# Performance work log

Measured on AMD Instinct MI355X. Metric: run time of the kernel, lower is better.

The kernel has to match this reference:

```python
import jax, jax.numpy as jnp
import numpy as np

O_DIM, A_DIM, Z_DIM = 256, 8, 9
D, H, L, M, B = 128, 128, 4, 4, 65536  # module dim, MLP hidden, n_layers, n_modules, batch


def setup_inputs() -> dict:
    key = jax.random.key(0)
    ks = jax.random.split(key, 18)
    s = 0.05
    return {
        "o": jax.random.normal(ks[0], (B, O_DIM), jnp.float32),
        "z_map": jax.random.uniform(ks[1], (B, Z_DIM), jnp.float32),
        "collision_prob": jax.random.uniform(ks[2], (B, 1), jnp.float32),
        # base obs embedding and routing (task) embedding
        "Wb": jax.random.normal(ks[3], (O_DIM, D), jnp.float32) * s,
        "bb": jnp.zeros((D,), jnp.float32),
        "Wz": jax.random.normal(ks[4], (Z_DIM + 1, D), jnp.float32) * s,
        "bz": jnp.zeros((D,), jnp.float32),
        # L layers x M modules of DxD linears
        "Wm": jax.random.normal(ks[5], (L, M, D, D), jnp.float32) * s,
        "bm": jnp.zeros((L, M, D), jnp.float32),
        # routing heads: L-1 inter-layer (M*M) gates + final (M,) gate
        "Wg": jax.random.normal(ks[6], (L - 1, D, M * M), jnp.float32) * s,
        "Wg_last": jax.random.normal(ks[7], (D, M), jnp.float32) * s,
        # dueling heads
        "Wv": jax.random.normal(ks[8], (D, 1), jnp.float32) * s,
        "bv": jnp.zeros((1,), jnp.float32),
        "Wa1": jax.random.normal(ks[9], (D, H), jnp.float32) * s,
        "ba1": jnp.zeros((H,), jnp.float32),
        "Wa2": jax.random.normal(ks[10], (H, A_DIM), jnp.float32) * s,
        "ba2": jnp.zeros((A_DIM,), jnp.float32),
    }


def _softmodule(o, z_map, collision_prob, Wb, bb, Wz, bz, Wm, bm, Wg, Wg_last):
    f0 = jax.nn.relu(o @ Wb + bb)                              # (B, D)
    z_in = jnp.concatenate([z_map, collision_prob], axis=-1)   # (B, Z+1)
    g = jax.nn.relu(z_in @ Wz + bz) * f0                       # routing embedding (B, D)
    # layer 0: all modules consume the obs embedding
    x = jax.nn.relu(jnp.einsum("bd,mde->bme", f0, Wm[0]) + bm[0])  # (B, M, D)
    for l in range(1, L):
        logits = (g @ Wg[l - 1]).reshape(-1, M, M)             # (B, i, j)
        p = jax.nn.softmax(logits, axis=1)                     # soft routing over incoming modules i
        xin = jnp.einsum("bij,bid->bjd", p, x)                 # weighted gather-combine
        x = jax.nn.relu(jnp.einsum("bmd,mde->bme", xin, Wm[l]) + bm[l])
    p_last = jax.nn.softmax(g @ Wg_last, axis=-1)              # (B, M)
    return jnp.einsum("bm,bmd->bd", p_last, x)                 # (B, D)


def reference(o, z_map, collision_prob, Wb, bb, Wz, bz, Wm, bm, Wg, Wg_last,
              Wv, bv, Wa1, ba1, Wa2, ba2):
    feature = _softmodule(o, z_map, collision_prob, Wb, bb, Wz, bz, Wm, bm, Wg, Wg_last)
    value = feature @ Wv + bv                                  # (B, 1)
    adv = jax.nn.relu(feature @ Wa1 + ba1) @ Wa2 + ba2         # (B, A)
    adv = adv - adv.mean(axis=-1, keepdims=True)
    return adv + value
```

## Files before the change

kernel.cpp:

```cpp
#include <hip/hip_runtime.h>
#include <stdint.h>


typedef __attribute__((ext_vector_type(8))) short short8;
typedef __attribute__((ext_vector_type(4))) float f32x4;
typedef __attribute__((ext_vector_type(2))) float f32x2;
typedef __attribute__((address_space(1))) const unsigned int u32_g;
typedef __attribute__((address_space(3))) unsigned int u32_l;

__device__ __forceinline__ unsigned short f2bf(float f) {
  union { float f; uint32_t u; } v; v.f = f;
  uint32_t r = v.u + 0x7FFFu + ((v.u >> 16) & 1u);
  return (unsigned short)(r >> 16);
}
__device__ __forceinline__ float blo(uint32_t w) { union { uint32_t u; float f; } c; c.u = w << 16; return c.f; }
__device__ __forceinline__ float bhi(uint32_t w) { union { uint32_t u; float f; } c; c.u = w & 0xffff0000u; return c.f; }
__device__ __forceinline__ float b2f(unsigned short h) { union { uint32_t u; float f; } c; c.u = ((uint32_t)h) << 16; return c.f; }
__device__ __forceinline__ uint32_t packrne(float lo, float hi) {
  union { float f; uint32_t u; } a, b; a.f = lo; b.f = hi;
  uint32_t ra = a.u + 0x7fffu + ((a.u >> 16) & 1u);
  uint32_t rb = b.u + 0x7fffu + ((b.u >> 16) & 1u);
  return (ra >> 16) | (rb & 0xffff0000u);
}
__device__ __forceinline__ f32x2 unpk2(uint32_t w) {
  f32x2 r; r.x = blo(w); r.y = bhi(w); return r;
}
union S8 { short8 s; uint32_t u[4]; };

__global__ void prep_weights(const float* __restrict__ Wb, const float* __restrict__ Wm,
                             const float* __restrict__ Wa1, const float* __restrict__ Wg,
                             const float* __restrict__ Wgl, const float* __restrict__ Wa2,
                             unsigned short* __restrict__ ws) {
  int idx = blockIdx.x * 256 + threadIdx.x;
  if (idx >= 321536) return;
  unsigned short v;
  if (idx < 32768) {
    int st = idx >> 12, n = (idx >> 5) & 127, kk = idx & 31;
    v = f2bf(Wb[(st * 32 + kk) * 128 + n]);
  } else if (idx < 40960) {
    int t = idx - 32768; int st = t >> 11, n = (t >> 5) & 63, kk = t & 31;
    int k = st * 32 + kk;
    if (n < 48)      v = f2bf(Wg[(n >> 4) * 2048 + k * 16 + (n & 15)]);
    else if (n < 52) v = f2bf(Wgl[k * 4 + (n - 48)]);
    else             v = 0;
  } else if (idx < 303104) {
    int t = idx - 40960; int lj = t >> 14; int g = t & 16383;
    int st = g >> 12, n = (g >> 5) & 127, kk = g & 31;
    v = f2bf(Wm[lj * 16384 + (st * 32 + kk) * 128 + n]);
  } else if (idx < 319488) {
    int t = idx - 303104; int st = t >> 12, n = (t >> 5) & 127, kk = t & 31;
    v = f2bf(Wa1[(st * 32 + kk) * 128 + n]);
  } else {
    int t = idx - 319488; int st = t >> 9, n = (t >> 5) & 15, kk = t & 31;
    v = (n < 8) ? f2bf(Wa2[(st * 32 + kk) * 8 + n]) : (unsigned short)0;
  }
  ws[idx] = v;
}

__device__ __forceinline__ void gld16(const void* g, void* l) {
  __builtin_amdgcn_global_load_lds((u32_g*)g, (u32_l*)l, 16, 0, 0);
}

__device__ __forceinline__ void gemm32(const short8 xst, const unsigned short* C,
                                       int q, int ml, f32x4 a[8]) {
#pragma unroll
  for (int nt = 0; nt < 8; ++nt) {
    short8 bf = *(const short8*)(C + (nt * 16 + ml) * 32 + q * 8);
    a[nt] = __builtin_amdgcn_mfma_f32_16x16x32_bf16(xst, bf, a[nt], 0, 0, 0);
  }
}

__device__ __forceinline__ void combine_layer(const short8 xo[4][4],
                                              const unsigned short* __restrict__ prow,
                                              short8 xin[4][4]) {
  float p[4][4];
#pragma unroll
  for (int j = 0; j < 4; ++j) {
    uint32_t pw0 = *(const uint32_t*)(prow + j * 4);
    uint32_t pw1 = *(const uint32_t*)(prow + j * 4 + 2);
    p[j][0] = blo(pw0); p[j][1] = bhi(pw0); p[j][2] = blo(pw1); p[j][3] = bhi(pw1);
  }
#pragma unroll
  for (int st = 0; st < 4; ++st) {
    S8 x0, x1, x2, x3;
    x0.s = xo[0][st]; x1.s = xo[1][st]; x2.s = xo[2][st]; x3.s = xo[3][st];
    S8 r0, r1, r2, r3;
#pragma unroll
    for (int w = 0; w < 4; ++w) {
      f32x2 u0 = unpk2(x0.u[w]), u1 = unpk2(x1.u[w]), u2 = unpk2(x2.u[w]), u3 = unpk2(x3.u[w]);
      f32x2 s0 = p[0][0] * u0 + p[0][1] * u1 + p[0][2] * u2 + p[0][3] * u3;
      f32x2 s1 = p[1][0] * u0 + p[1][1] * u1 + p[1][2] * u2 + p[1][3] * u3;
      f32x2 s2 = p[2][0] * u0 + p[2][1] * u1 + p[2][2] * u2 + p[2][3] * u3;
      f32x2 s3 = p[3][0] * u0 + p[3][1] * u1 + p[3][2] * u2 + p[3][3] * u3;
      r0.u[w] = packrne(s0.x, s0.y); r1.u[w] = packrne(s1.x, s1.y);
      r2.u[w] = packrne(s2.x, s2.y); r3.u[w] = packrne(s3.x, s3.y);
    }
    xin[0][st] = r0.s; xin[1][st] = r1.s; xin[2][st] = r2.s; xin[3][st] = r3.s;
  }
}

#define RSYNC1() asm volatile("s_waitcnt vmcnt(1) lgkmcnt(0)\n\ts_barrier" ::: "memory")
#define RSYNC0() asm volatile("s_waitcnt vmcnt(0) lgkmcnt(0)\n\ts_barrier" ::: "memory")
#define RSTEP1(PTR) do { RSYNC1(); ring_issue(); (PTR) = ring_next(); } while (0)
#define RSTEP0(PTR) do { RSYNC0(); ring_issue(); (PTR) = ring_next(); } while (0)

__global__ __attribute__((amdgpu_flat_work_group_size(512, 512), amdgpu_waves_per_eu(4)))
void dueling_fused(
    const float* __restrict__ o, const float* __restrict__ zmap, const float* __restrict__ coll,
    const float* __restrict__ bb, const float* __restrict__ Wz, const float* __restrict__ bz,
    const float* __restrict__ bm, const float* __restrict__ Wv, const float* __restrict__ bv,
    const float* __restrict__ ba1, const float* __restrict__ ba2,
    const unsigned short* __restrict__ ws, float* __restrict__ out)
{
  __shared__ __align__(16) unsigned char smem[77824];
  unsigned short* xbuf  = (unsigned short*)(smem + 24576);
  unsigned short* pall  = (unsigned short*)(smem + 59392);
  float*          zbufF = (float*)(smem + 59392);
  float*          plast = (float*)(smem + 71680);
  float*          vbuf  = (float*)(smem + 71680);
  unsigned short* bmL   = (unsigned short*)(smem + 73728);

  const int tid = threadIdx.x;
  const int wv  = tid >> 6;
  const int lane = tid & 63;
  const int q   = lane >> 4;
  const int ml  = lane & 15;
  const int row0 = blockIdx.x * 128;
  unsigned short* xbw = xbuf + wv * 2176;

  for (int i = tid; i < 1280; i += 512) {
    if (i < 1152) { int r = i / 9, c = i - r * 9; zbufF[r * 12 + c] = zmap[(row0 + r) * 9 + c]; }
    else          { int r = i - 1152; zbufF[r * 12 + 9] = coll[row0 + r]; }
  }
  for (int i = tid; i < 2048; i += 512) bmL[i] = f2bf(bm[i]);

  short8 of[8];
  const float* orow = o + (size_t)(row0 + wv * 16 + ml) * 256;
#pragma unroll
  for (int st = 0; st < 8; ++st) {
    float4 v0 = *(const float4*)(orow + st * 32 + q * 8);
    float4 v1 = *(const float4*)(orow + st * 32 + q * 8 + 4);
    S8 af;
    af.u[0] = packrne(v0.x, v0.y); af.u[1] = packrne(v0.z, v0.w);
    af.u[2] = packrne(v1.x, v1.y); af.u[3] = packrne(v1.z, v1.w);
    of[st] = af.s;
  }
  asm volatile("s_waitcnt vmcnt(0) lgkmcnt(0)" ::: "memory");

  int r_kiss = 0, r_riss = 0, r_rc = 0;
  const char* r_gsrc = (const char*)ws;
  const int wld  = wv << 10;
  const int ln16 = (tid & 63) << 4;
  auto ring_issue = [&]() {
    if (r_kiss <= 78) {
      char* l = (char*)smem + r_riss;
      int soff = (r_kiss == 78) ? (wld & 4095) : wld;
      gld16(r_gsrc + soff + ln16, l + wld + ln16);
      r_gsrc += 8192;
    }
    ++r_kiss;
    r_riss += 8192; if (r_riss == 24576) r_riss = 0;
  };
  auto ring_next = [&]() -> const unsigned short* {
    const unsigned short* p = (const unsigned short*)(smem + r_rc);
    r_rc += 8192; if (r_rc == 24576) r_rc = 0;
    return p;
  };
  ring_issue(); ring_issue();

  const f32x4 z4 = {0.f, 0.f, 0.f, 0.f};
  const unsigned short* C;

  f32x4 acc[8];
#pragma unroll
  for (int nt = 0; nt < 8; ++nt) acc[nt] = z4;
#pragma unroll
  for (int st = 0; st < 8; ++st) { RSTEP1(C); gemm32(of[st], C, q, ml, acc); }
#pragma unroll
  for (int nt = 0; nt < 8; ++nt) {
    float bbv = bb[nt * 16 + ml];
#pragma unroll
    for (int r2 = 0; r2 < 4; ++r2) {
      float v = fmaxf(acc[nt][r2] + bbv, 0.f);
      acc[nt][r2] = v;
      xbw[(q * 4 + r2) * 136 + nt * 16 + ml] = f2bf(v);
    }
  }
  short8 f0f[4];
#pragma unroll
  for (int st = 0; st < 4; ++st) f0f[st] = *(const short8*)(xbw + ml * 136 + st * 32 + q * 8);

#pragma unroll
  for (int nt = 0; nt < 8; ++nt) {
    int col = nt * 16 + ml;
    float wz[10];
#pragma unroll
    for (int k = 0; k < 10; ++k) wz[k] = Wz[k * 128 + col];
    float bzv = bz[col];
#pragma unroll
    for (int r2 = 0; r2 < 4; ++r2) {
      int row = wv * 16 + q * 4 + r2;
      float zd = bzv;
#pragma unroll
      for (int k = 0; k < 10; ++k) zd += zbufF[row * 12 + k] * wz[k];
      xbw[(q * 4 + r2) * 136 + col] = f2bf(fmaxf(zd, 0.f) * acc[nt][r2]);
    }
  }
  short8 gf[4];
#pragma unroll
  for (int st = 0; st < 4; ++st) gf[st] = *(const short8*)(xbw + ml * 136 + st * 32 + q * 8);

#pragma unroll
  for (int nt = 0; nt < 4; ++nt) acc[nt] = z4;
  RSTEP0(C);
#pragma unroll
  for (int sp = 0; sp < 2; ++sp)
#pragma unroll
    for (int nt = 0; nt < 4; ++nt) {
      short8 bf = *(const short8*)(C + (sp * 64 + nt * 16 + ml) * 32 + q * 8);
      acc[nt] = __builtin_amdgcn_mfma_f32_16x16x32_bf16(gf[sp], bf, acc[nt], 0, 0, 0);
    }
  RSTEP1(C);
#pragma unroll
  for (int sp = 0; sp < 2; ++sp)
#pragma unroll
    for (int nt = 0; nt < 4; ++nt) {
      short8 bf = *(const short8*)(C + (sp * 64 + nt * 16 + ml) * 32 + q * 8);
      acc[nt] = __builtin_amdgcn_mfma_f32_16x16x32_bf16(gf[2 + sp], bf, acc[nt], 0, 0, 0);
    }
#pragma unroll
  for (int li = 0; li < 3; ++li) {
#pragma unroll
    for (int r2 = 0; r2 < 4; ++r2) {
      float a = acc[li][r2];
      float m = fmaxf(a, __shfl_xor(a, 4)); m = fmaxf(m, __shfl_xor(m, 8));
      float e = __expf(a - m);
      float s = e; s += __shfl_xor(s, 4); s += __shfl_xor(s, 8);
      pall[(li * 128 + wv * 16 + q * 4 + r2) * 16 + (ml & 3) * 4 + (ml >> 2)] = f2bf(e / s);
    }
  }
#pragma unroll
  for (int r2 = 0; r2 < 4; ++r2) {
    float a = acc[3][r2];
    float m = fmaxf(a, __shfl_xor(a, 1)); m = fmaxf(m, __shfl_xor(m, 2));
    float e = __expf(a - m);
    float s = e; s += __shfl_xor(s, 1); s += __shfl_xor(s, 2);
    if (ml < 4) plast[(wv * 16 + q * 4 + r2) * 4 + ml] = e / s;
  }

  short8 xo[4][4];
  f32x4 a[8];
#pragma unroll
  for (int j = 0; j < 4; ++j) {
    if (j > 0) {
#pragma unroll
      for (int st = 0; st < 4; ++st) xo[j - 1][st] = *(const short8*)(xbw + ml * 136 + st * 32 + q * 8);
    }
#pragma unroll
    for (int nt = 0; nt < 8; ++nt) a[nt] = z4;
#pragma unroll
    for (int st = 0; st < 4; ++st) { RSTEP1(C); gemm32(f0f[st], C, q, ml, a); }
#pragma unroll
    for (int nt = 0; nt < 8; ++nt) {
      float bmv = b2f(bmL[j * 128 + nt * 16 + ml]);
#pragma unroll
      for (int r2 = 0; r2 < 4; ++r2)
        xbw[(q * 4 + r2) * 136 + nt * 16 + ml] = f2bf(fmaxf(a[nt][r2] + bmv, 0.f));
    }
  }

  short8 xin[4][4];
  for (int l = 1; l <= 2; ++l) {
#pragma unroll
    for (int st = 0; st < 4; ++st) xo[3][st] = *(const short8*)(xbw + ml * 136 + st * 32 + q * 8);
    combine_layer(xo, pall + ((l - 1) * 128 + wv * 16 + ml) * 16, xin);
#pragma unroll
    for (int j = 0; j < 4; ++j) {
      if (j > 0) {
#pragma unroll
        for (int st = 0; st < 4; ++st) xo[j - 1][st] = *(const short8*)(xbw + ml * 136 + st * 32 + q * 8);
      }
#pragma unroll
      for (int nt = 0; nt < 8; ++nt) a[nt] = z4;
#pragma unroll
      for (int st = 0; st < 4; ++st) { RSTEP1(C); gemm32(xin[j][st], C, q, ml, a); }
#pragma unroll
      for (int nt = 0; nt < 8; ++nt) {
        float bmv = b2f(bmL[(l * 4 + j) * 128 + nt * 16 + ml]);
#pragma unroll
        for (int r2 = 0; r2 < 4; ++r2)
          xbw[(q * 4 + r2) * 136 + nt * 16 + ml] = f2bf(fmaxf(a[nt][r2] + bmv, 0.f));
      }
    }
  }

  f32x4 feat[8];
  {
#pragma unroll
    for (int st = 0; st < 4; ++st) xo[3][st] = *(const short8*)(xbw + ml * 136 + st * 32 + q * 8);
    combine_layer(xo, pall + (2 * 128 + wv * 16 + ml) * 16, xin);
#pragma unroll
    for (int nt = 0; nt < 8; ++nt) feat[nt] = z4;
#pragma unroll
    for (int j = 0; j < 4; ++j) {
#pragma unroll
      for (int nt = 0; nt < 8; ++nt) a[nt] = z4;
#pragma unroll
      for (int st = 0; st < 4; ++st) { RSTEP1(C); gemm32(xin[j][st], C, q, ml, a); }
      float pl[4];
#pragma unroll
      for (int r2 = 0; r2 < 4; ++r2) pl[r2] = plast[(wv * 16 + q * 4 + r2) * 4 + j];
#pragma unroll
      for (int nt = 0; nt < 8; ++nt) {
        float bmv = b2f(bmL[(12 + j) * 128 + nt * 16 + ml]);
#pragma unroll
        for (int r2 = 0; r2 < 4; ++r2)
          feat[nt][r2] += pl[r2] * fmaxf(a[nt][r2] + bmv, 0.f);
      }
    }
  }

#pragma unroll
  for (int nt = 0; nt < 8; ++nt)
#pragma unroll
    for (int r2 = 0; r2 < 4; ++r2)
      xbw[(q * 4 + r2) * 136 + nt * 16 + ml] = f2bf(feat[nt][r2]);
  short8 ff[4];
#pragma unroll
  for (int st = 0; st < 4; ++st) ff[st] = *(const short8*)(xbw + ml * 136 + st * 32 + q * 8);
#pragma unroll
  for (int nt = 0; nt < 8; ++nt) a[nt] = z4;
#pragma unroll
  for (int st = 0; st < 4; ++st) { RSTEP1(C); gemm32(ff[st], C, q, ml, a); }

  {
    float wvv[8];
#pragma unroll
    for (int nt = 0; nt < 8; ++nt) wvv[nt] = Wv[nt * 16 + ml];
    float bvv = bv[0];
#pragma unroll
    for (int r2 = 0; r2 < 4; ++r2) {
      float v = 0.f;
#pragma unroll
      for (int nt = 0; nt < 8; ++nt) v += feat[nt][r2] * wvv[nt];
      v += __shfl_xor(v, 1); v += __shfl_xor(v, 2); v += __shfl_xor(v, 4); v += __shfl_xor(v, 8);
      if (ml == 0) vbuf[wv * 16 + q * 4 + r2] = v + bvv;
    }
  }

#pragma unroll
  for (int nt = 0; nt < 8; ++nt) {
    float b1v = ba1[nt * 16 + ml];
#pragma unroll
    for (int r2 = 0; r2 < 4; ++r2)
      xbw[(q * 4 + r2) * 136 + nt * 16 + ml] = f2bf(fmaxf(a[nt][r2] + b1v, 0.f));
  }
  short8 a1f[4];
#pragma unroll
  for (int st = 0; st < 4; ++st) a1f[st] = *(const short8*)(xbw + ml * 136 + st * 32 + q * 8);

  RSTEP0(C);
  f32x4 av = z4;
#pragma unroll
  for (int st = 0; st < 4; ++st) {
    short8 bf = *(const short8*)(C + (st * 16 + ml) * 32 + q * 8);
    av = __builtin_amdgcn_mfma_f32_16x16x32_bf16(a1f[st], bf, av, 0, 0, 0);
  }
  float ba2v = ba2[ml & 7];
#pragma unroll
  for (int r2 = 0; r2 < 4; ++r2) {
    float aa = av[r2] + ba2v;
    float s = aa + __shfl_xor(aa, 1); s += __shfl_xor(s, 2); s += __shfl_xor(s, 4);
    if (ml < 8)
      out[(size_t)(row0 + wv * 16 + q * 4 + r2) * 8 + ml] = aa - s * 0.125f + vbuf[wv * 16 + q * 4 + r2];
  }
}

extern "C" void kernel_launch(void* const* d_in, const int* in_sizes, int n_in,
                              void* d_out, int out_size, void* d_ws, size_t ws_size,
                              hipStream_t stream) {
  const float* o   = (const float*)d_in[0];
  const float* zm  = (const float*)d_in[1];
  const float* cp  = (const float*)d_in[2];
  const float* Wb  = (const float*)d_in[3];
  const float* bb  = (const float*)d_in[4];
  const float* Wz  = (const float*)d_in[5];
  const float* bz  = (const float*)d_in[6];
  const float* Wm  = (const float*)d_in[7];
  const float* bm  = (const float*)d_in[8];
  const float* Wg  = (const float*)d_in[9];
  const float* Wgl = (const float*)d_in[10];
  const float* Wv  = (const float*)d_in[11];
  const float* bv  = (const float*)d_in[12];
  const float* Wa1 = (const float*)d_in[13];
  const float* ba1 = (const float*)d_in[14];
  const float* Wa2 = (const float*)d_in[15];
  const float* ba2 = (const float*)d_in[16];
  unsigned short* wsT = (unsigned short*)d_ws;

  int B = in_sizes[0] / 256;

  hipLaunchKernelGGL(prep_weights, dim3(1256), dim3(256), 0, stream,
                     Wb, Wm, Wa1, Wg, Wgl, Wa2, wsT);
  hipLaunchKernelGGL(dueling_fused, dim3(B / 128), dim3(512), 0, stream,
                     o, zm, cp, bb, Wz, bz, bm, Wv, bv, ba1, ba2,
                     wsT, (float*)d_out);
}
```

Baseline: 223.9 us.

## Repack weight tiles to conflict-free LDS layout, use hardware bf16 pack, relax occupancy

Weight staging tiles are reordered so each quad's 8-element K slice sits contiguously across the 16 columns. B-fragment LDS reads then hit consecutive addresses and should avoid the bank conflicts of the old 32-element row stride. The manual round-to-nearest-even bf16 packing is replaced by the v_cvt_pk_bf16_f32 instruction. waves_per_eu is lowered from 4 to 2, giving the compiler more registers at the cost of an occupancy hint. A few repeated LDS fragment loads are also folded into a helper, which is only cleanup.

```diff
diff --git a/kernel.cpp b/kernel.cpp
--- a/kernel.cpp
+++ b/kernel.cpp
@@ -16,11 +16,10 @@
 __device__ __forceinline__ float blo(uint32_t w) { union { uint32_t u; float f; } c; c.u = w << 16; return c.f; }
 __device__ __forceinline__ float bhi(uint32_t w) { union { uint32_t u; float f; } c; c.u = w & 0xffff0000u; return c.f; }
 __device__ __forceinline__ float b2f(unsigned short h) { union { uint32_t u; float f; } c; c.u = ((uint32_t)h) << 16; return c.f; }
-__device__ __forceinline__ uint32_t packrne(float lo, float hi) {
-  union { float f; uint32_t u; } a, b; a.f = lo; b.f = hi;
-  uint32_t ra = a.u + 0x7fffu + ((a.u >> 16) & 1u);
-  uint32_t rb = b.u + 0x7fffu + ((b.u >> 16) & 1u);
-  return (ra >> 16) | (rb & 0xffff0000u);
+__device__ __forceinline__ uint32_t cvtpk(float lo, float hi) {
+  uint32_t d;
+  asm("v_cvt_pk_bf16_f32 %0, %1, %2" : "=v"(d) : "v"(lo), "v"(hi));
+  return d;
 }
 __device__ __forceinline__ f32x2 unpk2(uint32_t w) {
   f32x2 r; r.x = blo(w); r.y = bhi(w); return r;
@@ -35,24 +34,25 @@
   if (idx >= 321536) return;
   unsigned short v;
   if (idx < 32768) {
-    int st = idx >> 12, n = (idx >> 5) & 127, kk = idx & 31;
-    v = f2bf(Wb[(st * 32 + kk) * 128 + n]);
+    int st = idx >> 12, q = (idx >> 10) & 3, n = (idx >> 3) & 127, kk = idx & 7;
+    v = f2bf(Wb[(st * 32 + q * 8 + kk) * 128 + n]);
   } else if (idx < 40960) {
-    int t = idx - 32768; int st = t >> 11, n = (t >> 5) & 63, kk = t & 31;
-    int k = st * 32 + kk;
+    int t = idx - 32768; int st = t >> 11, q = (t >> 9) & 3, n = (t >> 3) & 63, kk = t & 7;
+    int k = st * 32 + q * 8 + kk;
     if (n < 48)      v = f2bf(Wg[(n >> 4) * 2048 + k * 16 + (n & 15)]);
     else if (n < 52) v = f2bf(Wgl[k * 4 + (n - 48)]);
     else             v = 0;
   } else if (idx < 303104) {
-    int t = idx - 40960; int lj = t >> 14; int g = t & 16383;
-    int st = g >> 12, n = (g >> 5) & 127, kk = g & 31;
-    v = f2bf(Wm[lj * 16384 + (st * 32 + kk) * 128 + n]);
+    int t = idx - 40960; int pg = t >> 12; int lj = pg >> 2, st = pg & 3;
+    int q = (t >> 10) & 3, n = (t >> 3) & 127, kk = t & 7;
+    v = f2bf(Wm[lj * 16384 + (st * 32 + q * 8 + kk) * 128 + n]);
   } else if (idx < 319488) {
-    int t = idx - 303104; int st = t >> 12, n = (t >> 5) & 127, kk = t & 31;
-    v = f2bf(Wa1[(st * 32 + kk) * 128 + n]);
+    int t = idx - 303104; int st = t >> 12, q = (t >> 10) & 3, n = (t >> 3) & 127, kk = t & 7;
+    v = f2bf(Wa1[(st * 32 + q * 8 + kk) * 128 + n]);
   } else {
-    int t = idx - 319488; int st = t >> 9, n = (t >> 5) & 15, kk = t & 31;
-    v = (n < 8) ? f2bf(Wa2[(st * 32 + kk) * 8 + n]) : (unsigned short)0;
+    int t = idx - 319488; int st = t >> 9, q = (t >> 7) & 3, n = (t >> 3) & 15, kk = t & 7;
+    int k = st * 32 + q * 8 + kk;
+    v = (n < 8) ? f2bf(Wa2[k * 8 + n]) : (unsigned short)0;
   }
   ws[idx] = v;
 }
@@ -65,9 +65,13 @@
                                        int q, int ml, f32x4 a[8]) {
 #pragma unroll
   for (int nt = 0; nt < 8; ++nt) {
-    short8 bf = *(const short8*)(C + (nt * 16 + ml) * 32 + q * 8);
+    short8 bf = *(const short8*)(C + q * 1024 + (nt * 16 + ml) * 8);
     a[nt] = __builtin_amdgcn_mfma_f32_16x16x32_bf16(xst, bf, a[nt], 0, 0, 0);
   }
+}
+__device__ __forceinline__ void ldx4(const unsigned short* xbw, int q, int ml, short8 f[4]) {
+#pragma unroll
+  for (int st = 0; st < 4; ++st) f[st] = *(const short8*)(xbw + ml * 136 + st * 32 + q * 8);
 }
 
 __device__ __forceinline__ void combine_layer(const short8 xo[4][4],
@@ -92,8 +96,8 @@
       f32x2 s1 = p[1][0] * u0 + p[1][1] * u1 + p[1][2] * u2 + p[1][3] * u3;
       f32x2 s2 = p[2][0] * u0 + p[2][1] * u1 + p[2][2] * u2 + p[2][3] * u3;
       f32x2 s3 = p[3][0] * u0 + p[3][1] * u1 + p[3][2] * u2 + p[3][3] * u3;
-      r0.u[w] = packrne(s0.x, s0.y); r1.u[w] = packrne(s1.x, s1.y);
-      r2.u[w] = packrne(s2.x, s2.y); r3.u[w] = packrne(s3.x, s3.y);
+      r0.u[w] = cvtpk(s0.x, s0.y); r1.u[w] = cvtpk(s1.x, s1.y);
+      r2.u[w] = cvtpk(s2.x, s2.y); r3.u[w] = cvtpk(s3.x, s3.y);
     }
     xin[0][st] = r0.s; xin[1][st] = r1.s; xin[2][st] = r2.s; xin[3][st] = r3.s;
   }
@@ -104,7 +108,7 @@
 #define RSTEP1(PTR) do { RSYNC1(); ring_issue(); (PTR) = ring_next(); } while (0)
 #define RSTEP0(PTR) do { RSYNC0(); ring_issue(); (PTR) = ring_next(); } while (0)
 
-__global__ __attribute__((amdgpu_flat_work_group_size(512, 512), amdgpu_waves_per_eu(4)))
+__global__ __attribute__((amdgpu_flat_work_group_size(512, 512), amdgpu_waves_per_eu(2)))
 void dueling_fused(
     const float* __restrict__ o, const float* __restrict__ zmap, const float* __restrict__ coll,
     const float* __restrict__ bb, const float* __restrict__ Wz, const float* __restrict__ bz,
@@ -141,8 +145,8 @@
     float4 v0 = *(const float4*)(orow + st * 32 + q * 8);
     float4 v1 = *(const float4*)(orow + st * 32 + q * 8 + 4);
     S8 af;
-    af.u[0] = packrne(v0.x, v0.y); af.u[1] = packrne(v0.z, v0.w);
-    af.u[2] = packrne(v1.x, v1.y); af.u[3] = packrne(v1.z, v1.w);
+    af.u[0] = cvtpk(v0.x, v0.y); af.u[1] = cvtpk(v0.z, v0.w);
+    af.u[2] = cvtpk(v1.x, v1.y); af.u[3] = cvtpk(v1.z, v1.w);
     of[st] = af.s;
   }
   asm volatile("s_waitcnt vmcnt(0) lgkmcnt(0)" ::: "memory");
@@ -187,8 +191,7 @@
     }
   }
   short8 f0f[4];
-#pragma unroll
-  for (int st = 0; st < 4; ++st) f0f[st] = *(const short8*)(xbw + ml * 136 + st * 32 + q * 8);
+  ldx4(xbw, q, ml, f0f);
 
 #pragma unroll
   for (int nt = 0; nt < 8; ++nt) {
@@ -207,32 +210,32 @@
     }
   }
   short8 gf[4];
-#pragma unroll
-  for (int st = 0; st < 4; ++st) gf[st] = *(const short8*)(xbw + ml * 136 + st * 32 + q * 8);
-
-#pragma unroll
-  for (int nt = 0; nt < 4; ++nt) acc[nt] = z4;
+  ldx4(xbw, q, ml, gf);
+
+  f32x4 ag[4];
+#pragma unroll
+  for (int nt = 0; nt < 4; ++nt) ag[nt] = z4;
   RSTEP0(C);
 #pragma unroll
   for (int sp = 0; sp < 2; ++sp)
 #pragma unroll
     for (int nt = 0; nt < 4; ++nt) {
-      short8 bf = *(const short8*)(C + (sp * 64 + nt * 16 + ml) * 32 + q * 8);
-      acc[nt] = __builtin_amdgcn_mfma_f32_16x16x32_bf16(gf[sp], bf, acc[nt], 0, 0, 0);
+      short8 bf = *(const short8*)(C + sp * 2048 + q * 512 + (nt * 16 + ml) * 8);
+      ag[nt] = __builtin_amdgcn_mfma_f32_16x16x32_bf16(gf[sp], bf, ag[nt], 0, 0, 0);
     }
   RSTEP1(C);
 #pragma unroll
   for (int sp = 0; sp < 2; ++sp)
 #pragma unroll
     for (int nt = 0; nt < 4; ++nt) {
-      short8 bf = *(const short8*)(C + (sp * 64 + nt * 16 + ml) * 32 + q * 8);
-      acc[nt] = __builtin_amdgcn_mfma_f32_16x16x32_bf16(gf[2 + sp], bf, acc[nt], 0, 0, 0);
+      short8 bf = *(const short8*)(C + sp * 2048 + q * 512 + (nt * 16 + ml) * 8);
+      ag[nt] = __builtin_amdgcn_mfma_f32_16x16x32_bf16(gf[2 + sp], bf, ag[nt], 0, 0, 0);
     }
 #pragma unroll
   for (int li = 0; li < 3; ++li) {
 #pragma unroll
     for (int r2 = 0; r2 < 4; ++r2) {
-      float a = acc[li][r2];
+      float a = ag[li][r2];
       float m = fmaxf(a, __shfl_xor(a, 4)); m = fmaxf(m, __shfl_xor(m, 8));
       float e = __expf(a - m);
       float s = e; s += __shfl_xor(s, 4); s += __shfl_xor(s, 8);
@@ -241,7 +244,7 @@
   }
 #pragma unroll
   for (int r2 = 0; r2 < 4; ++r2) {
-    float a = acc[3][r2];
+    float a = ag[3][r2];
     float m = fmaxf(a, __shfl_xor(a, 1)); m = fmaxf(m, __shfl_xor(m, 2));
     float e = __expf(a - m);
     float s = e; s += __shfl_xor(s, 1); s += __shfl_xor(s, 2);
@@ -252,10 +255,7 @@
   f32x4 a[8];
 #pragma unroll
   for (int j = 0; j < 4; ++j) {
-    if (j > 0) {
-#pragma unroll
-      for (int st = 0; st < 4; ++st) xo[j - 1][st] = *(const short8*)(xbw + ml * 136 + st * 32 + q * 8);
-    }
+    if (j > 0) ldx4(xbw, q, ml, xo[j - 1]);
 #pragma unroll
     for (int nt = 0; nt < 8; ++nt) a[nt] = z4;
 #pragma unroll
@@ -271,15 +271,11 @@
 
   short8 xin[4][4];
   for (int l = 1; l <= 2; ++l) {
-#pragma unroll
-    for (int st = 0; st < 4; ++st) xo[3][st] = *(const short8*)(xbw + ml * 136 + st * 32 + q * 8);
+    ldx4(xbw, q, ml, xo[3]);
     combine_layer(xo, pall + ((l - 1) * 128 + wv * 16 + ml) * 16, xin);
 #pragma unroll
     for (int j = 0; j < 4; ++j) {
-      if (j > 0) {
-#pragma unroll
-        for (int st = 0; st < 4; ++st) xo[j - 1][st] = *(const short8*)(xbw + ml * 136 + st * 32 + q * 8);
-      }
+      if (j > 0) ldx4(xbw, q, ml, xo[j - 1]);
 #pragma unroll
       for (int nt = 0; nt < 8; ++nt) a[nt] = z4;
 #pragma unroll
@@ -296,8 +292,7 @@
 
   f32x4 feat[8];
   {
-#pragma unroll
-    for (int st = 0; st < 4; ++st) xo[3][st] = *(const short8*)(xbw + ml * 136 + st * 32 + q * 8);
+    ldx4(xbw, q, ml, xo[3]);
     combine_layer(xo, pall + (2 * 128 + wv * 16 + ml) * 16, xin);
 #pragma unroll
     for (int nt = 0; nt < 8; ++nt) feat[nt] = z4;
@@ -326,8 +321,7 @@
     for (int r2 = 0; r2 < 4; ++r2)
       xbw[(q * 4 + r2) * 136 + nt * 16 + ml] = f2bf(feat[nt][r2]);
   short8 ff[4];
-#pragma unroll
-  for (int st = 0; st < 4; ++st) ff[st] = *(const short8*)(xbw + ml * 136 + st * 32 + q * 8);
+  ldx4(xbw, q, ml, ff);
 #pragma unroll
   for (int nt = 0; nt < 8; ++nt) a[nt] = z4;
 #pragma unroll
@@ -356,14 +350,13 @@
       xbw[(q * 4 + r2) * 136 + nt * 16 + ml] = f2bf(fmaxf(a[nt][r2] + b1v, 0.f));
   }
   short8 a1f[4];
-#pragma unroll
-  for (int st = 0; st < 4; ++st) a1f[st] = *(const short8*)(xbw + ml * 136 + st * 32 + q * 8);
+  ldx4(xbw, q, ml, a1f);
 
   RSTEP0(C);
   f32x4 av = z4;
 #pragma unroll
   for (int st = 0; st < 4; ++st) {
-    short8 bf = *(const short8*)(C + (st * 16 + ml) * 32 + q * 8);
+    short8 bf = *(const short8*)(C + st * 512 + q * 128 + ml * 8);
     av = __builtin_amdgcn_mfma_f32_16x16x32_bf16(a1f[st], bf, av, 0, 0, 0);
   }
   float ba2v = ba2[ml & 7];
```

After: 220.4 us. About the same (-1.6%).
